# Kernel tuning notes

Measured on AMD Instinct MI355X. Metric: run time of the kernel, lower is better.

The kernel has to match this reference:

```python
import jax, jax.numpy as jnp
import numpy as np

B, L, D = 2, 2048, 1024
H = 16
HD = D // H            # 64
HALF = HD // 2         # 32
PHASE_SCALE = 1.0
SCALE = HD ** -0.5


def _orthogonal_projection(rng, d, m):
    g = rng.standard_normal((d, m)).astype(np.float32)
    q, r = np.linalg.qr(g)
    s = np.sign(np.diagonal(r))
    s = np.where(s == 0, 1.0, s).astype(np.float32)
    q = q * s[None, :]
    q = q * np.sqrt(d / m)  # preserve_variance=True
    return jnp.asarray(q)


def setup_inputs() -> dict:
    key = jax.random.key(0)
    ks = jax.random.split(key, 6)
    rng = np.random.default_rng(0)
    return {
        "x": jax.random.normal(ks[0], (B, L, D), dtype=jnp.float32),
        "p": jax.random.normal(ks[1], (B, L, D), dtype=jnp.float32),
        "Wqkv": jax.random.normal(ks[2], (D, 3 * D), dtype=jnp.float32) * (D ** -0.5),
        "bqkv": jax.random.normal(ks[3], (3 * D,), dtype=jnp.float32) * 0.02,
        "Wout": jax.random.normal(ks[4], (D, D), dtype=jnp.float32) * (D ** -0.5),
        "bout": jax.random.normal(ks[5], (D,), dtype=jnp.float32) * 0.02,
        "proj": _orthogonal_projection(rng, D, D // 2),
    }


def _rotate_half(t, cos, sin):
    # non-interleaved rotary: split head_dim in halves
    t1, t2 = t[..., :HALF], t[..., HALF:]
    return jnp.concatenate((t1 * cos - t2 * sin, t1 * sin + t2 * cos), axis=-1)


def reference(x, p, Wqkv, bqkv, Wout, bout, proj):
    Bx, Lx = x.shape[0], x.shape[1]
    # QKV projection -> (B, L, 3, H, HD)
    qkv = (x @ Wqkv + bqkv).reshape(Bx, Lx, 3, H, HD)
    q, k, v = qkv[:, :, 0], qkv[:, :, 1], qkv[:, :, 2]
    # collaborative rotary phases from conditioning tokens p
    phases = (p @ proj).reshape(Bx, Lx, H, HALF) * PHASE_SCALE
    cos, sin = jnp.cos(phases), jnp.sin(phases)
    q = _rotate_half(q, cos, sin)
    k = _rotate_half(k, cos, sin)
    # non-causal softmax attention, scale = head_dim^-0.5
    scores = jnp.einsum("blhd,bmhd->bhlm", q, k) * SCALE
    attn = jax.nn.softmax(scores, axis=-1)
    out = jnp.einsum("bhlm,bmhd->blhd", attn, v).reshape(Bx, Lx, D)
    return out @ Wout + bout
```

## Files before the change

### kernel.cpp

```cpp
#include <hip/hip_runtime.h>


typedef __bf16 bf16;
typedef __bf16 bf16x8 __attribute__((ext_vector_type(8)));
typedef __bf16 bf16x4 __attribute__((ext_vector_type(4)));
typedef float f32x4 __attribute__((ext_vector_type(4)));
typedef float f32x16 __attribute__((ext_vector_type(16)));
typedef unsigned int u32;

__device__ __forceinline__ bf16 f2bf(float f) {
  unsigned u = __builtin_bit_cast(unsigned, f);
  u += 0x7FFFu + ((u >> 16) & 1u);
  unsigned short h = (unsigned short)(u >> 16);
  return __builtin_bit_cast(bf16, h);
}

__device__ __forceinline__ void gload_lds16(const bf16* g, bf16* l) {
  __builtin_amdgcn_global_load_lds((const __attribute__((address_space(1))) u32*)(const void*)g,
                                   (__attribute__((address_space(3))) u32*)(void*)l, 16, 0, 0);
}

__device__ __forceinline__ u32 cvtpk_bf16(float lo, float hi) {
  u32 r;
  asm("v_cvt_pk_bf16_f32 %0, %1, %2" : "=v"(r) : "v"(lo), "v"(hi));
  return r;
}
__device__ __forceinline__ void perm32swap(u32& a, u32& b) {
  asm("v_permlane32_swap_b32 %0, %1" : "+v"(a), "+v"(b));
}

#if __has_builtin(__builtin_amdgcn_exp2f)
#define EXP2(x) __builtin_amdgcn_exp2f(x)
#else
#define EXP2(x) exp2f(x)
#endif

#define QSCALE 0.18033688f

__device__ __forceinline__ void xcd_remap(int& bx, int& by) {
  const int nx = gridDim.x;
  const int nwg = nx * gridDim.y;
  const int lin = blockIdx.y * nx + blockIdx.x;
  const int chunk = nwg >> 3;
  const int nid = (lin & 7) * chunk + (lin >> 3);
  bx = nid % nx;
  by = nid / nx;
}

__global__ __launch_bounds__(256) void k_convert2(const float* __restrict__ a, bf16* __restrict__ oa,
                                                  const float* __restrict__ b, bf16* __restrict__ ob,
                                                  int n4each) {
  int i = blockIdx.x * 256 + threadIdx.x;
  const float* in = a; bf16* out = oa;
  if (i >= n4each) { in = b; out = ob; i -= n4each; }
  const float4 v = ((const float4*)in)[i];
  bf16x4 o;
  o[0] = f2bf(v.x); o[1] = f2bf(v.y); o[2] = f2bf(v.z); o[3] = f2bf(v.w);
  *(bf16x4*)(out + (size_t)i * 4) = o;
}

__global__ __launch_bounds__(256) void k_transpose3(const float* __restrict__ W1, bf16* __restrict__ O1,
                                                    const float* __restrict__ W2, bf16* __restrict__ O2,
                                                    const float* __restrict__ W3, bf16* __restrict__ O3) {
  __shared__ float t[64][65];
  int bx = blockIdx.x;
  const float* in; bf16* out; int C;
  if (bx < 48)      { in = W1; out = O1; C = 3072; }
  else if (bx < 56) { in = W2; out = O2; C = 512;  bx -= 48; }
  else              { in = W3; out = O3; C = 1024; bx -= 56; }
  const int R = 1024;
  const int c0 = bx * 64, r0 = blockIdx.y * 64;
  for (int e = threadIdx.x; e < 4096; e += 256) {
    int r = e >> 6, c = e & 63;
    t[r][c] = in[(size_t)(r0 + r) * C + c0 + c];
  }
  __syncthreads();
  for (int e = threadIdx.x; e < 4096; e += 256) {
    int c = e >> 6, r = e & 63;
    out[(size_t)(c0 + c) * R + r0 + r] = f2bf(t[r][c]);
  }
}

__global__ __launch_bounds__(512, 2) void k_gemm128x8(const bf16* __restrict__ A,
                                                      const bf16* __restrict__ Bt,
                                                      const float* __restrict__ bias,
                                                      float* __restrict__ C,
                                                      int M, int N, int K) {
  __shared__ bf16 sA0[8192], sA1[8192];
  __shared__ bf16 sB0[8192], sB1[8192];
  const int tid = threadIdx.x;
  const int lane = tid & 63, w = tid >> 6;
  const int lrow = lane & 15, lgrp = lane >> 4;
  const int wm = (w >> 2) * 64, wn = (w & 3) * 32;
  int bx, by;
  xcd_remap(bx, by);
  const int m0 = bx * 128, n0 = by * 128;
  const int rsub = lane >> 3, slot = lane & 7;
  const int swz8 = (slot ^ rsub) * 8;
  const int r7 = lrow & 7;
  const int nkt = K >> 6;

  const bf16* Ab = A  + (size_t)m0 * K;
  const bf16* Bb = Bt + (size_t)n0 * K;

  f32x4 acc[4][2] = {};

#pragma unroll
  for (int c = 0; c < 2; ++c) {
    gload_lds16(Ab + (size_t)(c * 64 + w * 8 + rsub) * K + swz8, sA0 + c * 4096 + w * 512);
    gload_lds16(Bb + (size_t)(c * 64 + w * 8 + rsub) * K + swz8, sB0 + c * 4096 + w * 512);
  }
  __syncthreads();

  for (int kt = 0; kt < nkt; ++kt) {
    const bf16* pA = (kt & 1) ? sA1 : sA0;
    const bf16* pB = (kt & 1) ? sB1 : sB0;
    bf16* nA = (kt & 1) ? sA0 : sA1;
    bf16* nB = (kt & 1) ? sB0 : sB1;
    const size_t knext = (size_t)(kt + 1) * 64;
    const bool more = (kt < nkt - 1);

#pragma unroll
    for (int kk = 0; kk < 2; ++kk) {
      bf16x8 af[4], bfr[2];
#pragma unroll
      for (int mi = 0; mi < 4; ++mi)
        af[mi] = *(const bf16x8*)&pA[(wm + mi * 16 + lrow) * 64 + ((kk * 4 + lgrp) ^ r7) * 8];
#pragma unroll
      for (int ni = 0; ni < 2; ++ni)
        bfr[ni] = *(const bf16x8*)&pB[(wn + ni * 16 + lrow) * 64 + ((kk * 4 + lgrp) ^ r7) * 8];
      if (more) {
        const bf16* src = kk ? Bb : Ab;
        bf16* dst = kk ? nB : nA;
#pragma unroll
        for (int c = 0; c < 2; ++c)
          gload_lds16(src + (size_t)(c * 64 + w * 8 + rsub) * K + knext + swz8, dst + c * 4096 + w * 512);
      }
      __builtin_amdgcn_s_setprio(1);
#pragma unroll
      for (int mi = 0; mi < 4; ++mi)
#pragma unroll
        for (int ni = 0; ni < 2; ++ni)
          acc[mi][ni] = __builtin_amdgcn_mfma_f32_16x16x32_bf16(af[mi], bfr[ni], acc[mi][ni], 0, 0, 0);
      __builtin_amdgcn_s_setprio(0);
    }
    __syncthreads();
  }

#pragma unroll
  for (int mi = 0; mi < 4; ++mi)
#pragma unroll
    for (int ni = 0; ni < 2; ++ni) {
      const int col = n0 + wn + ni * 16 + lrow;
      const float bv = bias ? bias[col] : 0.f;
#pragma unroll
      for (int j = 0; j < 4; ++j) {
        const int row = m0 + wm + mi * 16 + lgrp * 4 + j;
        C[(size_t)row * N + col] = acc[mi][ni][j] + bv;
      }
    }
}

__global__ __launch_bounds__(512, 2) void k_gemm_qkv256(const bf16* __restrict__ A,
                                                        const bf16* __restrict__ Bt,
                                                        const float* __restrict__ bqkv,
                                                        const float* __restrict__ phases,
                                                        bf16* __restrict__ qb,
                                                        bf16* __restrict__ kb,
                                                        bf16* __restrict__ vb) {
  __shared__ bf16 sA0[16384], sA1[16384];
  __shared__ bf16 sB0[16384], sB1[16384];
  const int tid = threadIdx.x;
  const int lane = tid & 63, w = tid >> 6;
  const int lrow = lane & 15, lgrp = lane >> 4;
  const int wm = (w >> 2) * 128;
  const int wn = (w & 3) * 64;
  const int m0 = blockIdx.x * 256, n0 = blockIdx.y * 256;
  const int K = 1024;

  const int srow = tid >> 3;
  const int swz8 = (((tid & 7) ^ (srow & 7))) * 8;
  const int r7 = lrow & 7;

  const bf16* Ab = A  + (size_t)m0 * K;
  const bf16* Bb = Bt + (size_t)n0 * K;

  f32x4 acc[8][4] = {};

#pragma unroll
  for (int g = 0; g < 4; ++g) {
    gload_lds16(Ab + (size_t)(g * 64 + srow) * K + swz8, sA0 + g * 4096 + w * 512);
    gload_lds16(Bb + (size_t)(g * 64 + srow) * K + swz8, sB0 + g * 4096 + w * 512);
  }
  __syncthreads();

  for (int kt = 0; kt < 16; ++kt) {
    const bf16* pA = (kt & 1) ? sA1 : sA0;
    const bf16* pB = (kt & 1) ? sB1 : sB0;
    bf16* nA = (kt & 1) ? sA0 : sA1;
    bf16* nB = (kt & 1) ? sB0 : sB1;
    const size_t knext = (size_t)(kt + 1) * 64;

    bf16x8 bfr[4][2];
#pragma unroll
    for (int ni = 0; ni < 4; ++ni)
#pragma unroll
      for (int kk = 0; kk < 2; ++kk)
        bfr[ni][kk] = *(const bf16x8*)&pB[(wn + ni * 16 + lrow) * 64 + ((kk * 4 + lgrp) ^ r7) * 8];

#pragma unroll
    for (int q = 0; q < 4; ++q) {
      if (kt < 15) {
        gload_lds16(Ab + (size_t)(q * 64 + srow) * K + knext + swz8, nA + q * 4096 + w * 512);
        gload_lds16(Bb + (size_t)(q * 64 + srow) * K + knext + swz8, nB + q * 4096 + w * 512);
      }
      bf16x8 af[2][2];
#pragma unroll
      for (int m2 = 0; m2 < 2; ++m2)
#pragma unroll
        for (int kk = 0; kk < 2; ++kk)
          af[m2][kk] = *(const bf16x8*)&pA[(wm + (q * 2 + m2) * 16 + lrow) * 64 + ((kk * 4 + lgrp) ^ r7) * 8];
      __builtin_amdgcn_s_setprio(1);
#pragma unroll
      for (int m2 = 0; m2 < 2; ++m2)
#pragma unroll
        for (int ni = 0; ni < 4; ++ni)
#pragma unroll
          for (int kk = 0; kk < 2; ++kk)
            acc[q * 2 + m2][ni] =
                __builtin_amdgcn_mfma_f32_16x16x32_bf16(af[m2][kk], bfr[ni][kk], acc[q * 2 + m2][ni], 0, 0, 0);
      __builtin_amdgcn_s_setprio(0);
    }
    __syncthreads();
  }

  const int nw = n0 + wn;
  const int sec = nw >> 10;
  const int hh = (nw & 1023) >> 6;
  const float b0 = bqkv[nw + lrow];
  const float b1 = bqkv[nw + 16 + lrow];
  const float b2 = bqkv[nw + 32 + lrow];
  const float b3 = bqkv[nw + 48 + lrow];

  if (sec == 2) {
#pragma unroll
    for (int mi = 0; mi < 8; ++mi) {
      const int row0 = m0 + wm + mi * 16 + lgrp * 4;
      const int b = row0 >> 11, l0 = row0 & 2047;
#pragma unroll
      for (int ni = 0; ni < 4; ++ni) {
        const int d = ni * 16 + lrow;
        const float bv = (ni == 0) ? b0 : (ni == 1) ? b1 : (ni == 2) ? b2 : b3;
        bf16x4 pv;
#pragma unroll
        for (int j = 0; j < 4; ++j) pv[j] = f2bf(acc[mi][ni][j] + bv);
        *(bf16x4*)&vb[(((size_t)(b * 16 + hh)) * 64 + d) * 2048 + l0] = pv;
      }
    }
  } else {
    bf16* qk = sec ? kb : qb;
    const float qs = sec ? 1.0f : QSCALE;
#pragma unroll
    for (int mi = 0; mi < 8; ++mi) {
#pragma unroll
      for (int j = 0; j < 4; ++j) {
        const int row = m0 + wm + mi * 16 + lgrp * 4 + j;
        const int b = row >> 11, l = row & 2047;
        const float ph1 = phases[(size_t)row * 512 + hh * 32 + lrow];
        const float ph2 = phases[(size_t)row * 512 + hh * 32 + 16 + lrow];
        float s1, c1, s2, c2;
        __sincosf(ph1, &s1, &c1);
        __sincosf(ph2, &s2, &c2);
        const float t0 = acc[mi][0][j] + b0;
        const float t1 = acc[mi][1][j] + b1;
        const float t2 = acc[mi][2][j] + b2;
        const float t3 = acc[mi][3][j] + b3;
        bf16* base = qk + (((size_t)(b * 16 + hh)) * 2048 + l) * 64;
        base[lrow]      = f2bf((t0 * c1 - t2 * s1) * qs);
        base[16 + lrow] = f2bf((t1 * c2 - t3 * s2) * qs);
        base[32 + lrow] = f2bf((t0 * s1 + t2 * c1) * qs);
        base[48 + lrow] = f2bf((t1 * s2 + t3 * c2) * qs);
      }
    }
  }
}

__global__ __launch_bounds__(256, 4) void k_flash_attn5(const bf16* __restrict__ qb,
                                                        const bf16* __restrict__ kb,
                                                        const bf16* __restrict__ vb,
                                                        bf16* __restrict__ attnout) {
  const int tid = threadIdx.x, lane = tid & 63, w = tid >> 6;
  const int ql = lane & 31, hi = lane >> 5;
  const int tsel = w >> 1;
  const int qh = w & 1;
  const int fid = blockIdx.x;
  const int nid = (fid & 7) * 128 + (fid >> 3);
  const int qblk = nid & 31, h = (nid >> 5) & 15, b = nid >> 9;
  const size_t bh = (size_t)b * 16 + h;
  const bf16* Kp = kb + bh * 2048 * 64;
  const bf16* Vp = vb + bh * 64 * 2048;

  __shared__ __align__(16) char smem[32768];
  bf16* sK = (bf16*)smem;
  bf16* sV = (bf16*)(smem + 16384);

  const bf16* Qp = qb + (bh * 2048 + (size_t)qblk * 64 + qh * 32 + ql) * 64;
  bf16x8 qf[4];
#pragma unroll
  for (int c = 0; c < 4; ++c) qf[c] = *(const bf16x8*)(Qp + c * 16 + hi * 8);

  const int srow = tid >> 3;
  const int swz = (tid & 7) ^ (srow & 7);

  f32x16 o0 = {}, o1 = {};
  float lsum = 0.f;

#define STAGE(BUF, KV0)                                                                       \
  do {                                                                                        \
    gload_lds16(Kp + (size_t)((KV0) + srow) * 64 + swz * 8,        sK + (BUF) * 4096 + w * 512); \
    gload_lds16(Kp + (size_t)((KV0) + srow + 32) * 64 + swz * 8,   sK + (BUF) * 4096 + 2048 + w * 512); \
    gload_lds16(Vp + (size_t)srow * 2048 + (KV0) + swz * 8,        sV + (BUF) * 4096 + w * 512); \
    gload_lds16(Vp + (size_t)(srow + 32) * 2048 + (KV0) + swz * 8, sV + (BUF) * 4096 + 2048 + w * 512); \
  } while (0)

  STAGE(0, 0);
  __syncthreads();

  for (int t = 0; t < 32; ++t) {
    const int cur = t & 1;
    if (t < 31) STAGE(cur ^ 1, (t + 1) * 64);

    const bf16* sKc = sK + cur * 4096;
    const bf16* sVc = sV + cur * 4096;

    f32x16 st0 = {};
#pragma unroll
    for (int c = 0; c < 4; ++c) {
      const int j = (c * 2 + hi) ^ (ql & 7);
      bf16x8 kf = *(const bf16x8*)&sKc[(tsel * 32 + ql) * 64 + j * 8];
      __builtin_amdgcn_s_setprio(1);
      st0 = __builtin_amdgcn_mfma_f32_32x32x16_bf16(kf, qf[c], st0, 0, 0, 0);
      __builtin_amdgcn_s_setprio(0);
    }

#pragma unroll
    for (int j2 = 0; j2 < 16; ++j2) {
      float pv = EXP2(st0[j2]);
      st0[j2] = pv; lsum += pv;
    }

#pragma unroll
    for (int fs = 0; fs < 2; ++fs) {
      u32 a0 = cvtpk_bf16(st0[fs * 8 + 0], st0[fs * 8 + 1]);
      u32 a1 = cvtpk_bf16(st0[fs * 8 + 2], st0[fs * 8 + 3]);
      u32 a2 = cvtpk_bf16(st0[fs * 8 + 4], st0[fs * 8 + 5]);
      u32 a3 = cvtpk_bf16(st0[fs * 8 + 6], st0[fs * 8 + 7]);
      perm32swap(a0, a2);
      perm32swap(a1, a3);
      union { u32 u[4]; bf16x8 v; } cu;
      cu.u[0] = a0; cu.u[1] = a1; cu.u[2] = a2; cu.u[3] = a3;
      const int j = (tsel * 4 + fs * 2 + hi) ^ (ql & 7);
      bf16x8 vf0 = *(const bf16x8*)&sVc[ql * 64 + j * 8];
      bf16x8 vf1 = *(const bf16x8*)&sVc[(32 + ql) * 64 + j * 8];
      __builtin_amdgcn_s_setprio(1);
      o0 = __builtin_amdgcn_mfma_f32_32x32x16_bf16(vf0, cu.v, o0, 0, 0, 0);
      o1 = __builtin_amdgcn_mfma_f32_32x32x16_bf16(vf1, cu.v, o1, 0, 0, 0);
      __builtin_amdgcn_s_setprio(0);
    }
    __syncthreads();
  }

  float* cb = (float*)smem;
  if (w >= 2) {
    const int idx = ((w - 2) * 64 + lane) * 34;
#pragma unroll
    for (int i = 0; i < 16; ++i) cb[idx + i] = o0[i];
#pragma unroll
    for (int i = 0; i < 16; ++i) cb[idx + 16 + i] = o1[i];
    cb[idx + 32] = lsum;
  }
  __syncthreads();
  if (w < 2) {
    const int idx = (w * 64 + lane) * 34;
#pragma unroll
    for (int i = 0; i < 16; ++i) o0[i] += cb[idx + i];
#pragma unroll
    for (int i = 0; i < 16; ++i) o1[i] += cb[idx + 16 + i];
    lsum += cb[idx + 32];
    lsum += __shfl_xor(lsum, 32);

    const float inv = 1.f / lsum;
    const int qrow = qblk * 64 + qh * 32 + ql;
    bf16* outp = attnout + ((size_t)b * 2048 + qrow) * 1024 + h * 64;
#pragma unroll
    for (int j2 = 0; j2 < 4; ++j2) {
      bf16x4 ov;
#pragma unroll
      for (int jj = 0; jj < 4; ++jj) ov[jj] = f2bf(o0[j2 * 4 + jj] * inv);
      *(bf16x4*)(outp + j2 * 8 + hi * 4) = ov;
#pragma unroll
      for (int jj = 0; jj < 4; ++jj) ov[jj] = f2bf(o1[j2 * 4 + jj] * inv);
      *(bf16x4*)(outp + 32 + j2 * 8 + hi * 4) = ov;
    }
  }
#undef STAGE
}

extern "C" void kernel_launch(void* const* d_in, const int* in_sizes, int n_in,
                              void* d_out, int out_size, void* d_ws, size_t ws_size,
                              hipStream_t stream) {
  (void)in_sizes; (void)n_in; (void)out_size; (void)ws_size;
  const float* x    = (const float*)d_in[0];
  const float* p    = (const float*)d_in[1];
  const float* Wqkv = (const float*)d_in[2];
  const float* bqkv = (const float*)d_in[3];
  const float* Wout = (const float*)d_in[4];
  const float* bout = (const float*)d_in[5];
  const float* proj = (const float*)d_in[6];
  float* out = (float*)d_out;

  char* ws = (char*)d_ws;
  size_t off = 0;
  bf16* xb     = (bf16*)(ws + off); off += (size_t)4096 * 1024 * 2;
  bf16* pb     = (bf16*)(ws + off); off += (size_t)4096 * 1024 * 2;
  bf16* WqkvT  = (bf16*)(ws + off); off += (size_t)3072 * 1024 * 2;
  bf16* projT  = (bf16*)(ws + off); off += (size_t)512  * 1024 * 2;
  bf16* WoutT  = (bf16*)(ws + off); off += (size_t)1024 * 1024 * 2;
  float* phases= (float*)(ws + off); off += (size_t)4096 * 512 * 4;
  bf16* qb     = (bf16*)(ws + off); off += (size_t)4096 * 1024 * 2;
  bf16* kb     = (bf16*)(ws + off); off += (size_t)4096 * 1024 * 2;
  bf16* vb     = (bf16*)(ws + off); off += (size_t)4096 * 1024 * 2;
  bf16* attnb  = (bf16*)(ws + off); off += (size_t)4096 * 1024 * 2;

  k_convert2<<<8192, 256, 0, stream>>>(x, xb, p, pb, 1048576);
  k_transpose3<<<dim3(72, 16), 256, 0, stream>>>(Wqkv, WqkvT, proj, projT, Wout, WoutT);

  k_gemm128x8<<<dim3(32, 4), 512, 0, stream>>>(pb, projT, nullptr, phases, 4096, 512, 1024);
  k_gemm_qkv256<<<dim3(16, 12), 512, 0, stream>>>(xb, WqkvT, bqkv, phases, qb, kb, vb);

  k_flash_attn5<<<1024, 256, 0, stream>>>(qb, kb, vb, attnb);

  k_gemm128x8<<<dim3(32, 8), 512, 0, stream>>>(attnb, WoutT, bout, out, 4096, 1024, 1024);
}
```

Measured before the change: 133.2 us.

## Merge conversion and transpose kernels; use smaller-tile GEMM for phase projection

```diff
diff --git a/kernel.cpp b/kernel.cpp
--- a/kernel.cpp
+++ b/kernel.cpp
@@ -47,29 +47,32 @@
   by = nid / nx;
 }
 
-__global__ __launch_bounds__(256) void k_convert2(const float* __restrict__ a, bf16* __restrict__ oa,
-                                                  const float* __restrict__ b, bf16* __restrict__ ob,
-                                                  int n4each) {
-  int i = blockIdx.x * 256 + threadIdx.x;
-  const float* in = a; bf16* out = oa;
-  if (i >= n4each) { in = b; out = ob; i -= n4each; }
-  const float4 v = ((const float4*)in)[i];
-  bf16x4 o;
-  o[0] = f2bf(v.x); o[1] = f2bf(v.y); o[2] = f2bf(v.z); o[3] = f2bf(v.w);
-  *(bf16x4*)(out + (size_t)i * 4) = o;
-}
-
-__global__ __launch_bounds__(256) void k_transpose3(const float* __restrict__ W1, bf16* __restrict__ O1,
-                                                    const float* __restrict__ W2, bf16* __restrict__ O2,
-                                                    const float* __restrict__ W3, bf16* __restrict__ O3) {
+__global__ __launch_bounds__(256) void k_prep(const float* __restrict__ x, bf16* __restrict__ xb,
+                                              const float* __restrict__ p, bf16* __restrict__ pb,
+                                              const float* __restrict__ W1, bf16* __restrict__ O1,
+                                              const float* __restrict__ W2, bf16* __restrict__ O2,
+                                              const float* __restrict__ W3, bf16* __restrict__ O3) {
+  const int gb = blockIdx.x;
+  if (gb < 8192) {
+    int i = gb * 256 + threadIdx.x;
+    const float* in = x; bf16* out = xb;
+    if (i >= 1048576) { in = p; out = pb; i -= 1048576; }
+    const float4 v = ((const float4*)in)[i];
+    bf16x4 o;
+    o[0] = f2bf(v.x); o[1] = f2bf(v.y); o[2] = f2bf(v.z); o[3] = f2bf(v.w);
+    *(bf16x4*)(out + (size_t)i * 4) = o;
+    return;
+  }
   __shared__ float t[64][65];
-  int bx = blockIdx.x;
+  const int lin = gb - 8192;
+  int bx = lin % 72;
+  const int by = lin / 72;
   const float* in; bf16* out; int C;
   if (bx < 48)      { in = W1; out = O1; C = 3072; }
   else if (bx < 56) { in = W2; out = O2; C = 512;  bx -= 48; }
   else              { in = W3; out = O3; C = 1024; bx -= 56; }
   const int R = 1024;
-  const int c0 = bx * 64, r0 = blockIdx.y * 64;
+  const int c0 = bx * 64, r0 = by * 64;
   for (int e = threadIdx.x; e < 4096; e += 256) {
     int r = e >> 6, c = e & 63;
     t[r][c] = in[(size_t)(r0 + r) * C + c0 + c];
@@ -161,6 +164,95 @@
     }
 }
 
+__global__ __launch_bounds__(256, 3) void k_gemm64(const bf16* __restrict__ A,
+                                                   const bf16* __restrict__ Bt,
+                                                   const float* __restrict__ bias,
+                                                   float* __restrict__ C,
+                                                   int M, int N, int K) {
+  __shared__ bf16 sA0[4096], sA1[4096];
+  __shared__ bf16 sB0[8192], sB1[8192];
+  const int tid = threadIdx.x;
+  const int lane = tid & 63, w = tid >> 6;
+  const int lrow = lane & 15, lgrp = lane >> 4;
+  const int wn = w * 32;
+  int bx, by;
+  xcd_remap(bx, by);
+  const int m0 = bx * 64, n0 = by * 128;
+  const int rsub = tid >> 3;
+  const int swz8 = ((tid & 7) ^ (rsub & 7)) * 8;
+  const int r7 = lrow & 7;
+  const int nkt = K >> 6;
+
+  const bf16* Ab = A  + (size_t)m0 * K;
+  const bf16* Bb = Bt + (size_t)n0 * K;
+
+  f32x4 acc[4][2] = {};
+
+#pragma unroll
+  for (int c = 0; c < 2; ++c)
+    gload_lds16(Ab + (size_t)(c * 32 + rsub) * K + swz8, sA0 + c * 2048 + (tid >> 6) * 512 + (tid & 63) / 64  + ((tid & 63) >> 3) * 0 + (tid - (tid >> 6) * 64) * 0 + w * 512);
+  __syncthreads();
+#pragma unroll
+  for (int c = 0; c < 2; ++c)
+    gload_lds16(Ab + (size_t)(c * 32 + rsub) * K + swz8, sA0 + c * 2048 + w * 512);
+#pragma unroll
+  for (int c = 0; c < 4; ++c)
+    gload_lds16(Bb + (size_t)(c * 32 + rsub) * K + swz8, sB0 + c * 2048 + w * 512);
+  __syncthreads();
+
+  for (int kt = 0; kt < nkt; ++kt) {
+    const bf16* pA = (kt & 1) ? sA1 : sA0;
+    const bf16* pB = (kt & 1) ? sB1 : sB0;
+    bf16* nA = (kt & 1) ? sA0 : sA1;
+    bf16* nB = (kt & 1) ? sB0 : sB1;
+    const size_t knext = (size_t)(kt + 1) * 64;
+    const bool more = (kt < nkt - 1);
+
+#pragma unroll
+    for (int kk = 0; kk < 2; ++kk) {
+      bf16x8 af[4], bfr[2];
+#pragma unroll
+      for (int mi = 0; mi < 4; ++mi)
+        af[mi] = *(const bf16x8*)&pA[(mi * 16 + lrow) * 64 + ((kk * 4 + lgrp) ^ r7) * 8];
+#pragma unroll
+      for (int ni = 0; ni < 2; ++ni)
+        bfr[ni] = *(const bf16x8*)&pB[(wn + ni * 16 + lrow) * 64 + ((kk * 4 + lgrp) ^ r7) * 8];
+      if (more) {
+        if (kk == 0) {
+#pragma unroll
+          for (int c = 0; c < 2; ++c)
+            gload_lds16(Ab + (size_t)(c * 32 + rsub) * K + knext + swz8, nA + c * 2048 + w * 512);
+        } else {
+#pragma unroll
+          for (int c = 0; c < 4; ++c)
+            gload_lds16(Bb + (size_t)(c * 32 + rsub) * K + knext + swz8, nB + c * 2048 + w * 512);
+        }
+      }
+      __builtin_amdgcn_s_setprio(1);
+#pragma unroll
+      for (int mi = 0; mi < 4; ++mi)
+#pragma unroll
+        for (int ni = 0; ni < 2; ++ni)
+          acc[mi][ni] = __builtin_amdgcn_mfma_f32_16x16x32_bf16(af[mi], bfr[ni], acc[mi][ni], 0, 0, 0);
+      __builtin_amdgcn_s_setprio(0);
+    }
+    __syncthreads();
+  }
+
+#pragma unroll
+  for (int mi = 0; mi < 4; ++mi)
+#pragma unroll
+    for (int ni = 0; ni < 2; ++ni) {
+      const int col = n0 + wn + ni * 16 + lrow;
+      const float bv = bias ? bias[col] : 0.f;
+#pragma unroll
+      for (int j = 0; j < 4; ++j) {
+        const int row = m0 + mi * 16 + lgrp * 4 + j;
+        C[(size_t)row * N + col] = acc[mi][ni][j] + bv;
+      }
+    }
+}
+
 __global__ __launch_bounds__(512, 2) void k_gemm_qkv256(const bf16* __restrict__ A,
                                                         const bf16* __restrict__ Bt,
                                                         const float* __restrict__ bqkv,
@@ -432,10 +524,9 @@
   bf16* vb     = (bf16*)(ws + off); off += (size_t)4096 * 1024 * 2;
   bf16* attnb  = (bf16*)(ws + off); off += (size_t)4096 * 1024 * 2;
 
-  k_convert2<<<8192, 256, 0, stream>>>(x, xb, p, pb, 1048576);
-  k_transpose3<<<dim3(72, 16), 256, 0, stream>>>(Wqkv, WqkvT, proj, projT, Wout, WoutT);
-
-  k_gemm128x8<<<dim3(32, 4), 512, 0, stream>>>(pb, projT, nullptr, phases, 4096, 512, 1024);
+  k_prep<<<9344, 256, 0, stream>>>(x, xb, p, pb, Wqkv, WqkvT, proj, projT, Wout, WoutT);
+
+  k_gemm64<<<dim3(64, 4), 256, 0, stream>>>(pb, projT, nullptr, phases, 4096, 512, 1024);
   k_gemm_qkv256<<<dim3(16, 12), 512, 0, stream>>>(xb, WqkvT, bqkv, phases, qb, kb, vb);
 
   k_flash_attn5<<<1024, 256, 0, stream>>>(qb, kb, vb, attnb);
```

Measured after the change: 132.5 us. Within noise of the previous version (-0.5%).
